# Performance work log

Measured on AMD Instinct MI355X. Metric: run time of the kernel, lower is better.

The kernel has to match this reference:

```python
import jax, jax.numpy as jnp
import numpy as np

N_HEADS = 16
ROPE_BASE = 10000.0


def _rotate_half(x):
    d = x.shape[-1] // 2
    return jnp.concatenate([-x[..., d:], x[..., :d]], axis=-1)


def _rope_tables(L, head_dim, dtype):
    inv_freq = 1.0 / (ROPE_BASE ** (jnp.arange(0, head_dim, 2, dtype=jnp.float32) / head_dim))
    t = jnp.arange(L, dtype=jnp.float32)
    freqs = jnp.outer(t, inv_freq)  # [L, head_dim//2]
    # torch code repeats cos/sin along last dim (tile x2) -> concat([c, c])
    cos = jnp.concatenate([jnp.cos(freqs), jnp.cos(freqs)], axis=-1).astype(dtype)
    sin = jnp.concatenate([jnp.sin(freqs), jnp.sin(freqs)], axis=-1).astype(dtype)
    return cos[None, None], sin[None, None]  # [1,1,L,head_dim]


def setup_inputs() -> dict:
    key = jax.random.key(0)
    kx, kq, kk, kv, ko = jax.random.split(key, 5)
    B, L, D = 4, 2048, 1024
    s = 0.02
    return {
        "x": jax.random.normal(kx, (B, L, D), dtype=jnp.float32),
        "Wq": jax.random.normal(kq, (D, D), dtype=jnp.float32) * s,
        "Wk": jax.random.normal(kk, (D, D), dtype=jnp.float32) * s,
        "Wv": jax.random.normal(kv, (D, D), dtype=jnp.float32) * s,
        "Wo": jax.random.normal(ko, (D, D), dtype=jnp.float32) * s,
    }


def reference(x, Wq, Wk, Wv, Wo):
    B, L, D = x.shape
    H = N_HEADS
    hd = D // H

    def split_heads(y):
        return y.reshape(B, L, H, hd).transpose(0, 2, 1, 3)  # [B,H,L,hd]

    q = split_heads(x @ Wq.T)
    k = split_heads(x @ Wk.T)
    v = split_heads(x @ Wv.T)

    cos, sin = _rope_tables(L, hd, x.dtype)
    q = q * cos + _rotate_half(q) * sin
    k = k * cos + _rotate_half(k) * sin

    scale = 1.0 / jnp.sqrt(jnp.asarray(hd, dtype=x.dtype))
    scores = jnp.einsum("bhqd,bhkd->bhqk", q, k) * scale
    attn = jax.nn.softmax(scores, axis=-1)
    out = jnp.einsum("bhqk,bhkd->bhqd", attn, v)
    out = out.transpose(0, 2, 1, 3).reshape(B, L, D)
    return out @ Wo.T
```

## Files before the change

kernel.cpp:

```cpp
#include <hip/hip_runtime.h>


typedef __bf16 bf16_t;
typedef __bf16 bf16x8 __attribute__((ext_vector_type(8)));
typedef __bf16 bf16x4 __attribute__((ext_vector_type(4)));
typedef float  floatx4 __attribute__((ext_vector_type(4)));
typedef unsigned int u32x2 __attribute__((ext_vector_type(2)));

#define B_  4
#define L_  2048
#define D_  1024
#define H_  16
#define HD_ 64
#define M_  (B_*L_)

__device__ __forceinline__ void async_copy16(const bf16_t* g, bf16_t* l) {
  __builtin_amdgcn_global_load_lds(
      (const __attribute__((address_space(1))) void*)g,
      (__attribute__((address_space(3))) void*)l, 16, 0, 0);
}

__device__ __forceinline__ unsigned int pack_bf16(float a, float b) {
  unsigned short ua = __builtin_bit_cast(unsigned short, (bf16_t)a);
  unsigned short ub = __builtin_bit_cast(unsigned short, (bf16_t)b);
  return (unsigned int)ua | ((unsigned int)ub << 16);
}

__global__ void prep_kernel(const float* __restrict__ x,
                            const float* __restrict__ wq, const float* __restrict__ wk,
                            const float* __restrict__ wv, const float* __restrict__ wo,
                            bf16_t* __restrict__ xb,
                            bf16_t* __restrict__ wqb, bf16_t* __restrict__ wkb,
                            bf16_t* __restrict__ wvb, bf16_t* __restrict__ wob,
                            float* __restrict__ cosT, float* __restrict__ sinT)
{
  const int NX = M_*D_;
  const int NW = D_*D_;
  int i = blockIdx.x*256 + threadIdx.x;
  if (i < NX) { xb[i] = (bf16_t)x[i]; return; }
  i -= NX;
  if (i < NW) { wqb[i] = (bf16_t)wq[i]; return; }
  i -= NW;
  if (i < NW) { wkb[i] = (bf16_t)wk[i]; return; }
  i -= NW;
  if (i < NW) { wvb[i] = (bf16_t)wv[i]; return; }
  i -= NW;
  if (i < NW) { wob[i] = (bf16_t)wo[i]; return; }
  i -= NW;
  if (i < L_*32) {
    int l = i >> 5, f = i & 31;
    double inv = pow(10000.0, -(double)f / 32.0);
    double ang = (double)l * inv;
    cosT[i] = (float)cos(ang);
    sinT[i] = (float)sin(ang);
  }
}

template<int MODE>
__global__ __launch_bounds__(256) void gemm_kernel(
    const bf16_t* __restrict__ A,
    const bf16_t* __restrict__ W0, const bf16_t* __restrict__ W1, const bf16_t* __restrict__ W2,
    bf16_t* __restrict__ C0, bf16_t* __restrict__ C1, bf16_t* __restrict__ C2,
    float* __restrict__ Cf,
    const float* __restrict__ cosT, const float* __restrict__ sinT)
{
  __shared__ __align__(16) bf16_t As[128*64];
  __shared__ __align__(16) bf16_t Bs[128*64];
  const int KD = 1024, ND = 1024;
  int z = (MODE==0) ? (int)blockIdx.z : 0;
  const bf16_t* W = (MODE==1) ? W0 : (z==0 ? W0 : (z==1 ? W1 : W2));
  int m0 = blockIdx.y*128, n0 = blockIdx.x*128;
  int tid = threadIdx.x;
  int wave = tid>>6, lane = tid&63, quad = lane>>4, lr = lane&15;
  int wm = wave>>1, wn = wave&1;
  int srow = lane>>3, sslot = lane&7;

  floatx4 zero4 = {0.f,0.f,0.f,0.f};
  floatx4 acc[4][4];
  #pragma unroll
  for (int i=0;i<4;i++)
    #pragma unroll
    for (int j=0;j<4;j++) acc[i][j] = zero4;

  #pragma unroll 1
  for (int k0 = 0; k0 < KD; k0 += 64) {
    #pragma unroll
    for (int j=0;j<4;j++) {
      int chunk = wave + j*4;
      int row = chunk*8 + srow;
      int col = ((sslot ^ (row&7)) << 3);
      async_copy16(A + (size_t)(m0+row)*KD + k0 + col, &As[chunk*512]);
      async_copy16(W + (size_t)(n0+row)*KD + k0 + col, &Bs[chunk*512]);
    }
    __syncthreads();
    #pragma unroll
    for (int ks=0; ks<2; ks++) {
      bf16x8 af[4], bfr[4];
      #pragma unroll
      for (int mi=0;mi<4;mi++)
        af[mi] = *(const bf16x8*)&As[(wm*64+mi*16+lr)*64 + (((ks*4+quad) ^ (lr&7))<<3)];
      #pragma unroll
      for (int ni=0;ni<4;ni++)
        bfr[ni] = *(const bf16x8*)&Bs[(wn*64+ni*16+lr)*64 + (((ks*4+quad) ^ (lr&7))<<3)];
      #pragma unroll
      for (int mi=0;mi<4;mi++)
        #pragma unroll
        for (int ni=0;ni<4;ni++)
          acc[mi][ni] = __builtin_amdgcn_mfma_f32_16x16x32_bf16(af[mi], bfr[ni], acc[mi][ni], 0,0,0);
    }
    __syncthreads();
  }

  if (MODE==1) {
    #pragma unroll
    for (int mi=0;mi<4;mi++) {
      int row = m0 + wm*64 + mi*16 + quad*4;
      #pragma unroll
      for (int ni=0;ni<4;ni++) {
        int col = n0 + wn*64 + ni*16 + lr;
        #pragma unroll
        for (int r=0;r<4;r++)
          Cf[(size_t)(row+r)*ND + col] = acc[mi][ni][r];
      }
    }
  } else if (z < 2) {
    bf16_t* Cb = (z==0) ? C0 : C1;
    const float sc = (z==0) ? 0.18033688011112042f : 1.0f;
    #pragma unroll
    for (int mi=0;mi<4;mi++) {
      int row = m0 + wm*64 + mi*16 + quad*4;
      int l = row & 2047;
      #pragma unroll
      for (int ni=0;ni<2;ni++) {
        int col = n0 + wn*64 + ni*16 + lr;
        int f = ni*16 + lr;
        #pragma unroll
        for (int r=0;r<4;r++) {
          float c = cosT[(l+r)*32 + f];
          float s = sinT[(l+r)*32 + f];
          float lo = acc[mi][ni][r], hi = acc[mi][ni+2][r];
          Cb[(size_t)(row+r)*ND + col]      = (bf16_t)((lo*c - hi*s)*sc);
          Cb[(size_t)(row+r)*ND + col + 32] = (bf16_t)((hi*c + lo*s)*sc);
        }
      }
    }
  } else {
    #pragma unroll
    for (int mi=0;mi<4;mi++) {
      int row0 = m0 + wm*64 + mi*16 + quad*4;
      int bb = row0 >> 11, ll = row0 & 2047;
      #pragma unroll
      for (int ni=0;ni<4;ni++) {
        int col = n0 + wn*64 + ni*16 + lr;
        int hh = col >> 6, dd = col & 63;
        uint2 val;
        val.x = pack_bf16(acc[mi][ni][0], acc[mi][ni][1]);
        val.y = pack_bf16(acc[mi][ni][2], acc[mi][ni][3]);
        *(uint2*)&C2[((size_t)((bb<<4)+hh)*64 + dd)*2048 + ll] = val;
      }
    }
  }
}

__global__ __launch_bounds__(256) void attn_kernel(
    const bf16_t* __restrict__ Q, const bf16_t* __restrict__ K,
    const bf16_t* __restrict__ Vt, bf16_t* __restrict__ O)
{
  __shared__ __align__(16) bf16_t Ks[3][4096];
  __shared__ __align__(16) bf16_t Vs[3][4096];
  int tid = threadIdx.x;
  int wave = tid>>6, lane = tid&63, quad = lane>>4, lr = lane&15;
  int bh = blockIdx.x; int b = bh>>4, h = bh&15;
  int q0 = blockIdx.y*128 + wave*32;
  size_t rowQ = (size_t)b*L_ + q0;

  int slr = (lr&3) | ((lr&4)<<1) | ((lr&8)>>1);

  int srow8 = lane>>3;
  int sslot = lane&7;

  bf16x8 qf[2][2];
  #pragma unroll
  for (int n=0;n<2;n++)
    #pragma unroll
    for (int ks=0;ks<2;ks++)
      qf[n][ks] = *(const bf16x8*)&Q[(rowQ + n*16 + lr)*D_ + h*HD_ + ks*32 + quad*8];

  const bf16_t* Kg = K + (size_t)b*L_*D_ + h*HD_;
  const bf16_t* Vg = Vt + (size_t)bh*HD_*L_;

  bf16x8 onesf;
  #pragma unroll
  for (int j=0;j<8;j++) onesf[j] = (bf16_t)1.0f;

  floatx4 zero4 = {0.f,0.f,0.f,0.f};
  floatx4 accO[2][4];
  floatx4 accS[2];
  accS[0] = zero4; accS[1] = zero4;
  #pragma unroll
  for (int n=0;n<2;n++)
    #pragma unroll
    for (int dt=0;dt<4;dt++) accO[n][dt] = zero4;

  auto stage = [&](int it, int c) {
    #pragma unroll
    for (int j=0;j<2;j++) {
      int row = wave*16 + j*8 + srow8;
      int col = ((sslot ^ (row&7)) << 3);
      async_copy16(Kg + (size_t)(it*64 + row)*D_ + col, &Ks[c][(wave*16 + j*8)*64]);
      async_copy16(Vg + (size_t)row*L_ + it*64 + col,   &Vs[c][(wave*16 + j*8)*64]);
    }
  };

  stage(0, 0);
  stage(1, 1);
  asm volatile("s_waitcnt vmcnt(4)" ::: "memory");
  __builtin_amdgcn_s_barrier();

  #pragma unroll 1
  for (int it = 0; it < 32; ++it) {
    int c = it % 3;
    if (it < 30) stage(it+2, (it+2) % 3);

    floatx4 St[2][4];
    #pragma unroll
    for (int t=0;t<4;t++) { St[0][t]=zero4; St[1][t]=zero4; }
    #pragma unroll
    for (int t=0;t<4;t++) {
      #pragma unroll
      for (int ks=0;ks<2;ks++) {
        bf16x8 kf = *(const bf16x8*)&Ks[c][(t*16+slr)*64 + (((ks*4+quad) ^ (slr&7))<<3)];
        St[0][t] = __builtin_amdgcn_mfma_f32_16x16x32_bf16(kf, qf[0][ks], St[0][t], 0,0,0);
        St[1][t] = __builtin_amdgcn_mfma_f32_16x16x32_bf16(kf, qf[1][ks], St[1][t], 0,0,0);
      }
    }

    bf16x8 pfv[2][2];
    #pragma unroll
    for (int n=0;n<2;n++) {
      #pragma unroll
      for (int hh=0;hh<2;hh++) {
        unsigned int w00 = pack_bf16(exp2f(St[n][2*hh][0]),   exp2f(St[n][2*hh][1]));
        unsigned int w01 = pack_bf16(exp2f(St[n][2*hh][2]),   exp2f(St[n][2*hh][3]));
        unsigned int w10 = pack_bf16(exp2f(St[n][2*hh+1][0]), exp2f(St[n][2*hh+1][1]));
        unsigned int w11 = pack_bf16(exp2f(St[n][2*hh+1][2]), exp2f(St[n][2*hh+1][3]));
        u32x2 r0 = __builtin_amdgcn_permlane32_swap(w00, w10, false, false);
        u32x2 r1 = __builtin_amdgcn_permlane32_swap(w01, w11, false, false);
        union { unsigned int u[4]; bf16x8 v; } pu;
        pu.u[0] = r0.x; pu.u[1] = r1.x; pu.u[2] = r0.y; pu.u[3] = r1.y;
        pfv[n][hh] = pu.v;
      }
    }

    #pragma unroll
    for (int dt=0;dt<4;dt++) {
      #pragma unroll
      for (int hh=0;hh<2;hh++) {
        bf16x8 vf = *(const bf16x8*)&Vs[c][(dt*16+lr)*64 + (((hh*4+quad) ^ (lr&7))<<3)];
        accO[0][dt] = __builtin_amdgcn_mfma_f32_16x16x32_bf16(vf, pfv[0][hh], accO[0][dt], 0,0,0);
        accO[1][dt] = __builtin_amdgcn_mfma_f32_16x16x32_bf16(vf, pfv[1][hh], accO[1][dt], 0,0,0);
      }
    }
    accS[0] = __builtin_amdgcn_mfma_f32_16x16x32_bf16(onesf, pfv[0][0], accS[0], 0,0,0);
    accS[1] = __builtin_amdgcn_mfma_f32_16x16x32_bf16(onesf, pfv[1][0], accS[1], 0,0,0);
    accS[0] = __builtin_amdgcn_mfma_f32_16x16x32_bf16(onesf, pfv[0][1], accS[0], 0,0,0);
    accS[1] = __builtin_amdgcn_mfma_f32_16x16x32_bf16(onesf, pfv[1][1], accS[1], 0,0,0);

    if (it < 30) {
      asm volatile("s_waitcnt vmcnt(4)" ::: "memory");
    } else {
      asm volatile("s_waitcnt vmcnt(0)" ::: "memory");
    }
    __builtin_amdgcn_s_barrier();
  }

  float inv0 = 1.0f / accS[0][0];
  float inv1 = 1.0f / accS[1][0];
  #pragma unroll
  for (int n=0;n<2;n++) {
    float inv = n ? inv1 : inv0;
    #pragma unroll
    for (int dt=0;dt<4;dt++) {
      uint2 w;
      w.x = pack_bf16(accO[n][dt][0]*inv, accO[n][dt][1]*inv);
      w.y = pack_bf16(accO[n][dt][2]*inv, accO[n][dt][3]*inv);
      *(uint2*)&O[(rowQ + n*16 + lr)*D_ + h*HD_ + dt*16 + quad*4] = w;
    }
  }
}

extern "C" void kernel_launch(void* const* d_in, const int* in_sizes, int n_in,
                              void* d_out, int out_size, void* d_ws, size_t ws_size,
                              hipStream_t stream) {
  const float* x  = (const float*)d_in[0];
  const float* wq = (const float*)d_in[1];
  const float* wk = (const float*)d_in[2];
  const float* wv = (const float*)d_in[3];
  const float* wo = (const float*)d_in[4];

  char* ws = (char*)d_ws;
  bf16_t* xb  = (bf16_t*)(ws);
  bf16_t* Qb  = (bf16_t*)(ws + (size_t)(16u<<20));
  bf16_t* Kb  = (bf16_t*)(ws + (size_t)(32u<<20));
  bf16_t* Vtb = (bf16_t*)(ws + (size_t)(48u<<20));
  bf16_t* wqb = (bf16_t*)(ws + (size_t)(64u<<20));
  bf16_t* wkb = (bf16_t*)(ws + (size_t)(66u<<20));
  bf16_t* wvb = (bf16_t*)(ws + (size_t)(68u<<20));
  bf16_t* wob = (bf16_t*)(ws + (size_t)(70u<<20));
  float* cosT = (float*)(ws + (size_t)(72u<<20));
  float* sinT = (float*)(ws + (size_t)(72u<<20) + (256u<<10));
  bf16_t* Ob = xb;

  prep_kernel<<<49408, 256, 0, stream>>>(x, wq, wk, wv, wo, xb, wqb, wkb, wvb, wob, cosT, sinT);
  gemm_kernel<0><<<dim3(8,64,3), 256, 0, stream>>>(xb, wqb, wkb, wvb, Qb, Kb, Vtb, nullptr, cosT, sinT);
  attn_kernel<<<dim3(64,16), 256, 0, stream>>>(Qb, Kb, Vtb, Ob);
  gemm_kernel<1><<<dim3(8,64,1), 256, 0, stream>>>(Ob, wob, nullptr, nullptr,
                                                   nullptr, nullptr, nullptr, (float*)d_out, cosT, sinT);
}
```

Baseline: 326.2 us.

## Triple-buffer GEMM K-loop with async LDS prefetch two tiles ahead

Replaces the single-buffered 64-wide K tile GEMM loop with a 3-stage ring of 32-wide K tiles. Global-to-LDS async copies for tile t+2 are issued before computing tile t, and a partial vmcnt wait plus one barrier per iteration replaces the two full syncthreads. This is meant to hide global load latency behind MFMA work. The cost is more loop iterations with half the MFMA work each, a narrower swizzle, and redundant reloads of the last tile near the end.

Result: slower. 353.1 us (+8.3%).

```diff
diff --git a/kernel.cpp b/kernel.cpp
--- a/kernel.cpp
+++ b/kernel.cpp
@@ -64,16 +64,18 @@
     float* __restrict__ Cf,
     const float* __restrict__ cosT, const float* __restrict__ sinT)
 {
-  __shared__ __align__(16) bf16_t As[128*64];
-  __shared__ __align__(16) bf16_t Bs[128*64];
+  __shared__ __align__(16) bf16_t SA[3][128*32];
+  __shared__ __align__(16) bf16_t SB[3][128*32];
   const int KD = 1024, ND = 1024;
+  const int NT = 32;
   int z = (MODE==0) ? (int)blockIdx.z : 0;
   const bf16_t* W = (MODE==1) ? W0 : (z==0 ? W0 : (z==1 ? W1 : W2));
   int m0 = blockIdx.y*128, n0 = blockIdx.x*128;
   int tid = threadIdx.x;
   int wave = tid>>6, lane = tid&63, quad = lane>>4, lr = lane&15;
   int wm = wave>>1, wn = wave&1;
-  int srow = lane>>3, sslot = lane&7;
+  int srow16 = lane>>2;
+  int sslot4 = lane&3;
 
   floatx4 zero4 = {0.f,0.f,0.f,0.f};
   floatx4 acc[4][4];
@@ -82,34 +84,46 @@
     #pragma unroll
     for (int j=0;j<4;j++) acc[i][j] = zero4;
 
+  auto stageA = [&](int ts, int c, int j) {
+    int row = j*64 + wave*16 + srow16;
+    int col = ((sslot4 ^ (row&3)) << 3);
+    async_copy16(A + (size_t)(m0+row)*KD + ts*32 + col, &SA[c][(j*64 + wave*16)*32]);
+  };
+  auto stageB = [&](int ts, int c, int j) {
+    int row = j*64 + wave*16 + srow16;
+    int col = ((sslot4 ^ (row&3)) << 3);
+    async_copy16(W + (size_t)(n0+row)*KD + ts*32 + col, &SB[c][(j*64 + wave*16)*32]);
+  };
+
+  stageA(0,0,0); stageA(0,0,1); stageB(0,0,0); stageB(0,0,1);
+  stageA(1,1,0); stageA(1,1,1); stageB(1,1,0); stageB(1,1,1);
+  asm volatile("s_waitcnt vmcnt(4)" ::: "memory");
+  __builtin_amdgcn_s_barrier();
+
   #pragma unroll 1
-  for (int k0 = 0; k0 < KD; k0 += 64) {
-    #pragma unroll
-    for (int j=0;j<4;j++) {
-      int chunk = wave + j*4;
-      int row = chunk*8 + srow;
-      int col = ((sslot ^ (row&7)) << 3);
-      async_copy16(A + (size_t)(m0+row)*KD + k0 + col, &As[chunk*512]);
-      async_copy16(W + (size_t)(n0+row)*KD + k0 + col, &Bs[chunk*512]);
-    }
-    __syncthreads();
-    #pragma unroll
-    for (int ks=0; ks<2; ks++) {
-      bf16x8 af[4], bfr[4];
-      #pragma unroll
-      for (int mi=0;mi<4;mi++)
-        af[mi] = *(const bf16x8*)&As[(wm*64+mi*16+lr)*64 + (((ks*4+quad) ^ (lr&7))<<3)];
+  for (int t = 0; t < NT; ++t) {
+    int c  = t % 3;
+    int cn = (t+2) % 3;
+    int ts = (t+2 < NT) ? (t+2) : (NT-1);
+    stageA(ts,cn,0); stageA(ts,cn,1); stageB(ts,cn,0); stageB(ts,cn,1);
+
+    bf16x8 af[4], bfr[4];
+    #pragma unroll
+    for (int mi=0;mi<4;mi++)
+      af[mi]  = *(const bf16x8*)&SA[c][(wm*64+mi*16+lr)*32 + ((quad^(lr&3))<<3)];
+    #pragma unroll
+    for (int ni=0;ni<4;ni++)
+      bfr[ni] = *(const bf16x8*)&SB[c][(wn*64+ni*16+lr)*32 + ((quad^(lr&3))<<3)];
+    #pragma unroll
+    for (int mi=0;mi<4;mi++)
       #pragma unroll
       for (int ni=0;ni<4;ni++)
-        bfr[ni] = *(const bf16x8*)&Bs[(wn*64+ni*16+lr)*64 + (((ks*4+quad) ^ (lr&7))<<3)];
-      #pragma unroll
-      for (int mi=0;mi<4;mi++)
-        #pragma unroll
-        for (int ni=0;ni<4;ni++)
-          acc[mi][ni] = __builtin_amdgcn_mfma_f32_16x16x32_bf16(af[mi], bfr[ni], acc[mi][ni], 0,0,0);
-    }
-    __syncthreads();
-  }
+        acc[mi][ni] = __builtin_amdgcn_mfma_f32_16x16x32_bf16(af[mi], bfr[ni], acc[mi][ni], 0,0,0);
+
+    asm volatile("s_waitcnt vmcnt(4)" ::: "memory");
+    __builtin_amdgcn_s_barrier();
+  }
+  asm volatile("s_waitcnt vmcnt(0)" ::: "memory");
 
   if (MODE==1) {
     #pragma unroll
@@ -175,7 +189,6 @@
   size_t rowQ = (size_t)b*L_ + q0;
 
   int slr = (lr&3) | ((lr&4)<<1) | ((lr&8)>>1);
-
   int srow8 = lane>>3;
   int sslot = lane&7;
 
```
